# Kernel optimization log

Hardware: AMD Instinct MI355X
Metric: run time of the kernel (lower is better)

## Reference

```python
import jax, jax.numpy as jnp
import numpy as np

# Production-scale dims: N tokens = 64 batch x 8192 seq, hidden width 256.
N, D_IN, D_OUT = 524288, 256, 256
P_NONZERO = 0.05  # mimics bnn.random.calc_desired_var -> sparse ternary W


def binarise(v):
    # bnn.functions.binarise forward: sign with binarise(0) = +1
    return jnp.where(v >= 0, 1.0, -1.0).astype(v.dtype)


def setup_inputs() -> dict:
    key = jax.random.key(0)
    kx, kw = jax.random.split(key)
    # x: binary activations in {-1,+1} (output of a previous binarise layer)
    x = jnp.where(jax.random.normal(kx, (N, D_IN)) >= 0, 1.0, -1.0).astype(jnp.float32)
    # W: ternary {-1, 0, +1} with Var = P_NONZERO (values +-1 each w.p. p/2)
    u = jax.random.uniform(kw, (D_IN, D_OUT))
    W = jnp.where(u < P_NONZERO / 2, -1.0,
                  jnp.where(u < P_NONZERO, 1.0, 0.0)).astype(jnp.float32)
    return {"x": x, "W": W}


def reference(x, W):
    # integer = x @ W  (ternary-weight matmul; int math in torch, same values in fp32)
    integer = x @ W  # [N, D_OUT]
    return binarise(integer)
```

## Files before the change

kernel.cpp:

```cpp
#include <hip/hip_runtime.h>
#include <stdint.h>


#define NROWS 524288
#define DDIM  256

__global__ __launch_bounds__(256, 4)
void ternbin_kernel(const float* __restrict__ x, const float* __restrict__ W,
                    float* __restrict__ out) {
    __shared__ uint32_t ldsP[DDIM][8];
    __shared__ uint32_t ldsM[DDIM][8];
    __shared__ int      ldsC[DDIM];

    const int t = threadIdx.x;

    {
        uint32_t P[8] = {0,0,0,0,0,0,0,0};
        uint32_t M[8] = {0,0,0,0,0,0,0,0};
        #pragma unroll 4
        for (int k = 0; k < DDIM; ++k) {
            float v = W[k * DDIM + t];
            int w = ((k & 3) << 1) | (k >> 7);
            uint32_t bit = 1u << ((k >> 2) & 31);
            if (v > 0.5f)       P[w] |= bit;
            else if (v < -0.5f) M[w] |= bit;
        }
        int c = 0;
        #pragma unroll
        for (int w = 0; w < 8; ++w) {
            ldsP[t][w] = P[w];
            ldsM[t][w] = M[w];
            c += __popc(P[w]) - __popc(M[w]);
        }
        ldsC[t] = c;
    }
    __syncthreads();

    const int lane = t & 63;
    uint32_t P[4][8], M[4][8];
    int C[4];
    #pragma unroll
    for (int jc = 0; jc < 4; ++jc) {
        const int col = 4 * lane + jc;
        #pragma unroll
        for (int w = 0; w < 8; ++w) {
            P[jc][w] = ldsP[col][w];
            M[jc][w] = ldsM[col][w];
        }
        C[jc] = ldsC[col];
    }
    __syncthreads();

    const int wave_in_block   = t >> 6;
    const int waves_per_block = blockDim.x >> 6;
    const int global_wave     = blockIdx.x * waves_per_block + wave_in_block;
    const int total_waves     = gridDim.x * waves_per_block;

    for (int row = global_wave; row < NROWS; row += total_waves) {
        const uint4 xv = *reinterpret_cast<const uint4*>(
            x + (size_t)row * DDIM + 4 * lane);
        const uint64_t b0 = __ballot((int)xv.x < 0);
        const uint64_t b1 = __ballot((int)xv.y < 0);
        const uint64_t b2 = __ballot((int)xv.z < 0);
        const uint64_t b3 = __ballot((int)xv.w < 0);
        uint32_t s[8];
        s[0] = (uint32_t)b0; s[1] = (uint32_t)(b0 >> 32);
        s[2] = (uint32_t)b1; s[3] = (uint32_t)(b1 >> 32);
        s[4] = (uint32_t)b2; s[5] = (uint32_t)(b2 >> 32);
        s[6] = (uint32_t)b3; s[7] = (uint32_t)(b3 >> 32);

        float4 o;
        float* op = &o.x;
        #pragma unroll
        for (int jc = 0; jc < 4; ++jc) {
            int accP = 0, accM = 0;
            #pragma unroll
            for (int w = 0; w < 8; ++w) {
                accP += __popc(s[w] & P[jc][w]);
                accM += __popc(s[w] & M[jc][w]);
            }
            const int diff = C[jc] + 2 * (accM - accP);
            op[jc] = (diff >= 0) ? 1.0f : -1.0f;
        }
        *reinterpret_cast<float4*>(out + (size_t)row * DDIM + 4 * lane) = o;
    }
}

extern "C" void kernel_launch(void* const* d_in, const int* in_sizes, int n_in,
                              void* d_out, int out_size, void* d_ws, size_t ws_size,
                              hipStream_t stream) {
    const float* x = (const float*)d_in[0];
    const float* W = (const float*)d_in[1];
    float* out = (float*)d_out;
    ternbin_kernel<<<2048, 256, 0, stream>>>(x, W, out);
}
```

Baseline: 1.136 ms.

## Batch four row loads per wave, use XOR-mask popcount and bitwise sign output

Each wave now owns a contiguous block of 64 rows and issues four 16-byte row loads before computing, which raises memory-level parallelism compared with one load per loop iteration. The ternary weights are re-encoded as a nonzero mask plus a sign mask, so each column needs one popcount of (s^M)&A per word instead of two popcounts. The ±1 output is built by OR-ing the sign bit into 1.0f rather than a compare and select. LDS rows are padded to 9 words and the occupancy hint drops to 3 blocks per SIMD to leave room for the extra registers. The contiguous per-wave mapping hardcodes a launch of 2048 blocks of 256 threads.

```diff
diff --git a/kernel.cpp b/kernel.cpp
--- a/kernel.cpp
+++ b/kernel.cpp
@@ -5,84 +5,92 @@
 #define NROWS 524288
 #define DDIM  256
 
-__global__ __launch_bounds__(256, 4)
+typedef uint32_t u32;
+typedef unsigned long long u64;
+
+__global__ __launch_bounds__(256, 3)
 void ternbin_kernel(const float* __restrict__ x, const float* __restrict__ W,
                     float* __restrict__ out) {
-    __shared__ uint32_t ldsP[DDIM][8];
-    __shared__ uint32_t ldsM[DDIM][8];
-    __shared__ int      ldsC[DDIM];
+    __shared__ u32 ldsA[DDIM][9];
+    __shared__ u32 ldsM[DDIM][9];
+    __shared__ int ldsC[DDIM];
 
     const int t = threadIdx.x;
 
     {
-        uint32_t P[8] = {0,0,0,0,0,0,0,0};
-        uint32_t M[8] = {0,0,0,0,0,0,0,0};
-        #pragma unroll 4
+        u32 A[8] = {0,0,0,0,0,0,0,0};
+        u32 M[8] = {0,0,0,0,0,0,0,0};
+        #pragma unroll 8
         for (int k = 0; k < DDIM; ++k) {
-            float v = W[k * DDIM + t];
-            int w = ((k & 3) << 1) | (k >> 7);
-            uint32_t bit = 1u << ((k >> 2) & 31);
-            if (v > 0.5f)       P[w] |= bit;
-            else if (v < -0.5f) M[w] |= bit;
+            const float v = W[k * DDIM + t];
+            const int   w = ((k & 3) << 1) | (k >> 7);
+            const u32 bit = 1u << ((k >> 2) & 31);
+            if (v != 0.0f) A[w] |= bit;
+            if (v <  0.0f) M[w] |= bit;
         }
         int c = 0;
         #pragma unroll
         for (int w = 0; w < 8; ++w) {
-            ldsP[t][w] = P[w];
+            ldsA[t][w] = A[w];
             ldsM[t][w] = M[w];
-            c += __popc(P[w]) - __popc(M[w]);
+            c += __popc(A[w]);
         }
         ldsC[t] = c;
     }
     __syncthreads();
 
     const int lane = t & 63;
-    uint32_t P[4][8], M[4][8];
+    u32 A[4][8], M[4][8];
     int C[4];
     #pragma unroll
     for (int jc = 0; jc < 4; ++jc) {
         const int col = 4 * lane + jc;
         #pragma unroll
         for (int w = 0; w < 8; ++w) {
-            P[jc][w] = ldsP[col][w];
+            A[jc][w] = ldsA[col][w];
             M[jc][w] = ldsM[col][w];
         }
         C[jc] = ldsC[col];
     }
     __syncthreads();
 
-    const int wave_in_block   = t >> 6;
-    const int waves_per_block = blockDim.x >> 6;
-    const int global_wave     = blockIdx.x * waves_per_block + wave_in_block;
-    const int total_waves     = gridDim.x * waves_per_block;
+    const int gwave = (int)((blockIdx.x * blockDim.x + (unsigned)t) >> 6);
+    const float* xp = x   + (size_t)gwave * 64 * DDIM + 4 * lane;
+    float*       op = out + (size_t)gwave * 64 * DDIM + 4 * lane;
 
-    for (int row = global_wave; row < NROWS; row += total_waves) {
-        const uint4 xv = *reinterpret_cast<const uint4*>(
-            x + (size_t)row * DDIM + 4 * lane);
-        const uint64_t b0 = __ballot((int)xv.x < 0);
-        const uint64_t b1 = __ballot((int)xv.y < 0);
-        const uint64_t b2 = __ballot((int)xv.z < 0);
-        const uint64_t b3 = __ballot((int)xv.w < 0);
-        uint32_t s[8];
-        s[0] = (uint32_t)b0; s[1] = (uint32_t)(b0 >> 32);
-        s[2] = (uint32_t)b1; s[3] = (uint32_t)(b1 >> 32);
-        s[4] = (uint32_t)b2; s[5] = (uint32_t)(b2 >> 32);
-        s[6] = (uint32_t)b3; s[7] = (uint32_t)(b3 >> 32);
+    #pragma unroll 1
+    for (int it = 0; it < 16; ++it) {
+        uint4 xv[4];
+        #pragma unroll
+        for (int rr = 0; rr < 4; ++rr)
+            xv[rr] = *reinterpret_cast<const uint4*>(xp + (size_t)(4 * it + rr) * DDIM);
 
-        float4 o;
-        float* op = &o.x;
         #pragma unroll
-        for (int jc = 0; jc < 4; ++jc) {
-            int accP = 0, accM = 0;
+        for (int rr = 0; rr < 4; ++rr) {
+            const u64 b0 = __ballot((int)xv[rr].x < 0);
+            const u64 b1 = __ballot((int)xv[rr].y < 0);
+            const u64 b2 = __ballot((int)xv[rr].z < 0);
+            const u64 b3 = __ballot((int)xv[rr].w < 0);
+            u32 s[8];
+            s[0] = (u32)b0; s[1] = (u32)(b0 >> 32);
+            s[2] = (u32)b1; s[3] = (u32)(b1 >> 32);
+            s[4] = (u32)b2; s[5] = (u32)(b2 >> 32);
+            s[6] = (u32)b3; s[7] = (u32)(b3 >> 32);
+
+            u32 o[4];
             #pragma unroll
-            for (int w = 0; w < 8; ++w) {
-                accP += __popc(s[w] & P[jc][w]);
-                accM += __popc(s[w] & M[jc][w]);
+            for (int jc = 0; jc < 4; ++jc) {
+                int p = 0;
+                #pragma unroll
+                for (int w = 0; w < 8; ++w)
+                    p += __popc((s[w] ^ M[jc][w]) & A[jc][w]);
+                const int d = C[jc] - 2 * p;
+                o[jc] = 0x3f800000u | ((u32)d & 0x80000000u);
             }
-            const int diff = C[jc] + 2 * (accM - accP);
-            op[jc] = (diff >= 0) ? 1.0f : -1.0f;
+            uint4 ov;
+            ov.x = o[0]; ov.y = o[1]; ov.z = o[2]; ov.w = o[3];
+            *reinterpret_cast<uint4*>(op + (size_t)(4 * it + rr) * DDIM) = ov;
         }
-        *reinterpret_cast<float4*>(out + (size_t)row * DDIM + 4 * lane) = o;
     }
 }
 
```

Measured after the change: 1.087 ms. -4.4%, faster.
